# Optimization experiments

Measured on AMD Instinct MI355X. Metric: run time of the kernel, lower is better.

Reference implementation:

```python
import jax, jax.numpy as jnp
import numpy as np

N = 100_000   # nodes
E = 1_600_000 # edges (avg degree 16)
D0, D1, D2 = 128, 64, 64


def _linp(key, n_out, n_in):
    kw, kb = jax.random.split(key)
    s = 1.0 / np.sqrt(n_in)
    W = jax.random.uniform(kw, (n_out, n_in), jnp.float32, -s, s)
    b = jax.random.uniform(kb, (n_out,), jnp.float32, -s, s)
    return W, b


def setup_inputs() -> dict:
    key = jax.random.key(0)
    ks = jax.random.split(key, 9)
    h = jax.random.normal(ks[0], (N, D0), jnp.float32)
    # guarantee every row has at least one edge (avoids empty-row softmax / 0-std NaNs)
    rows = jnp.concatenate([jnp.arange(N, dtype=jnp.int32),
                            jax.random.randint(ks[1], (E - N,), 0, N, jnp.int32)])
    cols = jax.random.randint(ks[2], (E,), 0, N, jnp.int32)
    edge_index = jnp.stack([rows, cols])  # [2, E], row = softmax segment
    W11, b11 = _linp(ks[3], D1, D0)
    W12, b12 = _linp(ks[4], 1, D1)
    W13, b13 = _linp(ks[5], D1, D0)
    W21, b21 = _linp(ks[6], D2, D1)
    W22, b22 = _linp(ks[7], 1, D2)
    W23, b23 = _linp(ks[8], D2, D1)
    return dict(h=h, edge_index=edge_index,
                W11=W11, b11=b11, W12=W12, b12=b12, W13=W13, b13=b13,
                W21=W21, b21=b21, W22=W22, b22=b22, W23=W23, b23=b23)


def reference(h, edge_index, W11, b11, W12, b12, W13, b13,
              W21, b21, W22, b22, W23, b23):
    src, dst = edge_index[0], edge_index[1]

    def gat_layer(x, Wa, ba, We, be, Wv, bv):
        a = jnp.tanh(x @ Wa.T + ba)                       # [N, d] node scores (l11/l21)
        e = jnp.tanh((a[src] + a[dst]) @ We.T + be)[:, 0] # [E] per-edge logit (l12/l22)
        # per-row (segment) softmax over src = row index
        m = jax.ops.segment_max(e, src, num_segments=N)
        ex = jnp.exp(e - m[src])
        denom = jax.ops.segment_sum(ex, src, num_segments=N)
        att = ex / denom[src]                             # [E]
        v = jnp.tanh(x @ Wv.T + bv)                       # [N, d] values (l13/l23)
        out = jax.ops.segment_sum(att[:, None] * v[dst], src, num_segments=N)  # sparse mm
        return out / jnp.std(out, -1, keepdims=True, ddof=1)  # torch.std is unbiased

    h = gat_layer(h, W11, b11, W12, b12, W13, b13)
    h = gat_layer(h, W21, b21, W22, b22, W23, b23)
    return h
```

## Files before the change

kernel.cpp:

```cpp
#include <hip/hip_runtime.h>


#define WS_ALIGN 256
#define BIN_SHIFT 7
#define BIN_NODES 128
#define BIN_CAP 2560
#define MAX_BINS 1024
#define EPB 4096

typedef __attribute__((ext_vector_type(8))) short short8;
typedef __attribute__((ext_vector_type(4))) float f32x4;

__device__ __forceinline__ float wave_sum(float x) {
#pragma unroll
  for (int m = 32; m > 0; m >>= 1) x += __shfl_xor(x, m, 64);
  return x;
}

__device__ __forceinline__ float fast_tanh(float x) {
  x = fminf(15.f, fmaxf(-15.f, x));
  float e = __expf(2.f * x);
  return (e - 1.f) * __builtin_amdgcn_rcpf(e + 1.f);
}

__device__ __forceinline__ unsigned short f32_to_bf16_rne(float f) {
  unsigned u = __float_as_uint(f);
  unsigned r = u + 0x7fffu + ((u >> 16) & 1u);
  return (unsigned short)(r >> 16);
}

__device__ __forceinline__ void prepw_one(const float* __restrict__ Wa,
                                          const float* __restrict__ Wv,
                                          short* __restrict__ Wh, short* __restrict__ Wl,
                                          int K, int i) {
  int KBLK = K / 32;
  int j = i & 7;
  int c = (i >> 3) & 15;
  int q = (i >> 7) & 3;
  int r = i >> 9;
  int nt = r / KBLK, kb = r - nt * KBLK;
  int row = nt * 16 + c;
  int col = kb * 32 + q * 8 + j;
  float f = (row < 64) ? Wa[row * K + col] : Wv[(row - 64) * K + col];
  unsigned u = __float_as_uint(f);
  float hf = __uint_as_float(u & 0xffff0000u);
  Wh[i] = (short)(u >> 16);
  Wl[i] = (short)(__float_as_uint(f - hf) >> 16);
}

__global__ void k_setup(const float* __restrict__ W11, const float* __restrict__ W13,
                        short* __restrict__ Wh1, short* __restrict__ Wl1,
                        const float* __restrict__ W21, const float* __restrict__ W23,
                        short* __restrict__ Wh2, short* __restrict__ Wl2,
                        int* __restrict__ cursor, int nb) {
  int i = blockIdx.x * 256 + threadIdx.x;
  if (i < 16384) {
    prepw_one(W11, W13, Wh1, Wl1, 128, i);
  } else if (i < 16384 + 8192) {
    prepw_one(W21, W23, Wh2, Wl2, 64, i - 16384);
  } else {
    int b = i - 24576;
    if (b < nb) cursor[b] = b * BIN_CAP;
  }
}

__global__ __launch_bounds__(256) void k_bin(const int* __restrict__ src,
                                             const int* __restrict__ dst,
                                             int* __restrict__ cursor,
                                             int* __restrict__ binned, int E, int nb) {
  __shared__ int ssrc[EPB];
  __shared__ int sdst[EPB];
  __shared__ int hist[MAX_BINS];
  __shared__ int base[MAX_BINS];
  int t = threadIdx.x;
  for (int i = t; i < nb; i += 256) hist[i] = 0;
  __syncthreads();
  int e0 = blockIdx.x * EPB;
  for (int i = t; i < EPB; i += 256) {
    int e = e0 + i;
    int sv = -1, dv = 0;
    if (e < E) {
      sv = src[e];
      dv = dst[e];
      atomicAdd(&hist[sv >> BIN_SHIFT], 1);
    }
    ssrc[i] = sv;
    sdst[i] = dv;
  }
  __syncthreads();
  for (int b = t; b < nb; b += 256) {
    int c = hist[b];
    base[b] = c ? atomicAdd(&cursor[b], c) : 0;
    hist[b] = 0;
  }
  __syncthreads();
  for (int i = t; i < EPB; i += 256) {
    int sv = ssrc[i];
    if (sv >= 0) {
      int b = sv >> BIN_SHIFT;
      int r = atomicAdd(&hist[b], 1);
      int pos = base[b] + r;
      if (pos < (b + 1) * BIN_CAP)
        binned[pos] = (sdst[i] << BIN_SHIFT) | (sv & (BIN_NODES - 1));
    }
  }
}

__global__ __launch_bounds__(256) void k_sort_bin(int* __restrict__ binned,
                                                  const int* __restrict__ cursor,
                                                  int* __restrict__ rs,
                                                  int* __restrict__ re, int n) {
  __shared__ int ents[BIN_CAP];
  __shared__ int sorted[BIN_CAP];
  __shared__ int hist[BIN_NODES];
  __shared__ int scan[BIN_NODES];
  __shared__ int cur[BIN_NODES];
  int bin = blockIdx.x;
  int t = threadIdx.x;
  int nbase = bin << BIN_SHIFT;
  int cnt = cursor[bin] - bin * BIN_CAP;
  if (cnt > BIN_CAP) cnt = BIN_CAP;
  if (t < BIN_NODES) hist[t] = 0;
  __syncthreads();
  int* bp = binned + (size_t)bin * BIN_CAP;
  for (int i = t; i < cnt; i += 256) {
    int pk = bp[i];
    ents[i] = pk;
    atomicAdd(&hist[pk & (BIN_NODES - 1)], 1);
  }
  __syncthreads();
  if (t < BIN_NODES) scan[t] = hist[t];
  __syncthreads();
  for (int off = 1; off < BIN_NODES; off <<= 1) {
    int add = (t < BIN_NODES && t >= off) ? scan[t - off] : 0;
    __syncthreads();
    if (t < BIN_NODES) scan[t] += add;
    __syncthreads();
  }
  if (t < BIN_NODES) {
    int ex = scan[t] - hist[t];
    cur[t] = ex;
    int node = nbase + t;
    if (node < n) {
      rs[node] = bin * BIN_CAP + ex;
      re[node] = bin * BIN_CAP + ex + hist[t];
    }
  }
  __syncthreads();
  for (int i = t; i < cnt; i += 256) {
    int pk = ents[i];
    int pos = atomicAdd(&cur[pk & (BIN_NODES - 1)], 1);
    sorted[pos] = pk;
  }
  __syncthreads();
  for (int i = t; i < cnt; i += 256) {
    int pk = sorted[i];
    int node = pk & (BIN_NODES - 1);
    int hi = scan[node];
    int lo = hi - hist[node];
    int r = lo;
    for (int j = lo; j < hi; j++) {
      int pj = sorted[j];
      r += (pj < pk) || (pj == pk && j < i);
    }
    ents[r] = pk >> BIN_SHIFT;
  }
  __syncthreads();
  for (int i = t; i < cnt; i += 256) bp[i] = ents[i];
}

template <int K>
__global__ __launch_bounds__(256) void k_node(
    const float* __restrict__ x, const short* __restrict__ Wh,
    const short* __restrict__ Wl, const float* __restrict__ ba,
    const float* __restrict__ we, const float* __restrict__ bv,
    unsigned short* __restrict__ v_out, float* __restrict__ s_out, int n) {
  constexpr int KBLK = K / 32;
  constexpr int KP = K + 4;
  __shared__ float sx[64 * KP];
  int t = threadIdx.x;
  int l = t & 63;
  int w = t >> 6;
  int q = l >> 4, c = l & 15;
  int node0b = blockIdx.x * 64;

  {
    const float4* xg = (const float4*)(x + (size_t)node0b * K);
    constexpr int R4 = K / 4;
#pragma unroll
    for (int it = 0; it < 64 * R4 / 256; it++) {
      int i = it * 256 + t;
      int r = i / R4, k4 = i - r * R4;
      float4 val = (node0b + r < n) ? xg[i] : (float4){0.f, 0.f, 0.f, 0.f};
      *(float4*)&sx[r * KP + k4 * 4] = val;
    }
  }
  __syncthreads();

  int node0w = node0b + w * 16;
  if (node0w >= n) return;

  const short8* WhF = (const short8*)Wh;
  const short8* WlF = (const short8*)Wl;

  f32x4 acc[8];
#pragma unroll
  for (int i = 0; i < 8; i++) acc[i] = (f32x4){0.f, 0.f, 0.f, 0.f};

  const float* xl = sx + (w * 16 + c) * KP;

#pragma unroll 1
  for (int kb = 0; kb < KBLK; kb++) {
    float4 x0 = *(const float4*)&xl[kb * 32 + q * 8];
    float4 x1 = *(const float4*)&xl[kb * 32 + q * 8 + 4];
    float xv[8] = {x0.x, x0.y, x0.z, x0.w, x1.x, x1.y, x1.z, x1.w};
    short8 ah, al;
#pragma unroll
    for (int j = 0; j < 8; j++) {
      unsigned u = __float_as_uint(xv[j]);
      ah[j] = (short)(u >> 16);
      float hf = __uint_as_float(u & 0xffff0000u);
      al[j] = (short)(__float_as_uint(xv[j] - hf) >> 16);
    }
#pragma unroll
    for (int nt = 0; nt < 8; nt++) {
      short8 wh = WhF[(size_t)(nt * KBLK + kb) * 64 + l];
      short8 wl = WlF[(size_t)(nt * KBLK + kb) * 64 + l];
      acc[nt] = __builtin_amdgcn_mfma_f32_16x16x32_bf16(ah, wh, acc[nt], 0, 0, 0);
      acc[nt] = __builtin_amdgcn_mfma_f32_16x16x32_bf16(ah, wl, acc[nt], 0, 0, 0);
      acc[nt] = __builtin_amdgcn_mfma_f32_16x16x32_bf16(al, wh, acc[nt], 0, 0, 0);
    }
  }

  float p[4] = {0.f, 0.f, 0.f, 0.f};
#pragma unroll
  for (int nt = 0; nt < 4; nt++) {
    int o = nt * 16 + c;
    float bav = ba[o], wev = we[o];
#pragma unroll
    for (int r = 0; r < 4; r++) p[r] += fast_tanh(acc[nt][r] + bav) * wev;
  }
#pragma unroll
  for (int mm = 1; mm < 16; mm <<= 1) {
#pragma unroll
    for (int r = 0; r < 4; r++) p[r] += __shfl_xor(p[r], mm, 64);
  }
  if (c == 0) {
#pragma unroll
    for (int r = 0; r < 4; r++) {
      int node = node0w + q * 4 + r;
      if (node < n) s_out[node] = p[r];
    }
  }
#pragma unroll
  for (int nt = 4; nt < 8; nt++) {
    int o = (nt - 4) * 16 + c;
    float bvv = bv[o];
#pragma unroll
    for (int r = 0; r < 4; r++) {
      int node = node0w + q * 4 + r;
      if (node < n)
        v_out[(size_t)node * 64 + o] = f32_to_bf16_rne(fast_tanh(acc[nt][r] + bvv));
    }
  }
}

__global__ __launch_bounds__(256) void k_aggr(const int* __restrict__ rs,
                                              const int* __restrict__ re,
                                              const int* __restrict__ col,
                                              const float* __restrict__ s,
                                              const float* __restrict__ be_p,
                                              const unsigned short* __restrict__ v,
                                              float* __restrict__ out, int n) {
  int gw = (int)((blockIdx.x * 256 + threadIdx.x) >> 6);
  int l = threadIdx.x & 63;
  if (gw >= n) return;
  int e0 = rs[gw], e1 = re[gw];
  float srow = s[gw];
  float be = be_p[0];
  int es = l >> 4;
  int g = l & 15;
  float a0 = 0.f, a1 = 0.f, a2 = 0.f, a3 = 0.f;
  float denom = 0.f;

  for (int base = e0; base < e1; base += 64) {
    int m = e1 - base;
    if (m > 64) m = 64;
    int c = 0;
    float w = 0.f;
    if (l < m) {
      c = col[base + l];
      w = __expf(fast_tanh(srow + s[c] + be));
    }
    denom += wave_sum(w);
    int iters = (m + 3) >> 2;
    for (int it = 0; it < iters; it++) {
      int j = (it << 2) + es;
      int cj = __shfl(c, j);
      float wj = __shfl(w, j);
      uint2 pk = *(const uint2*)(v + ((size_t)cj << 6) + (g << 2));
      a0 = fmaf(wj, __uint_as_float(pk.x << 16), a0);
      a1 = fmaf(wj, __uint_as_float(pk.x & 0xffff0000u), a1);
      a2 = fmaf(wj, __uint_as_float(pk.y << 16), a2);
      a3 = fmaf(wj, __uint_as_float(pk.y & 0xffff0000u), a3);
    }
  }

#pragma unroll
  for (int mm = 16; mm < 64; mm <<= 1) {
    a0 += __shfl_xor(a0, mm, 64);
    a1 += __shfl_xor(a1, mm, 64);
    a2 += __shfl_xor(a2, mm, 64);
    a3 += __shfl_xor(a3, mm, 64);
  }
  float inv = __builtin_amdgcn_rcpf(denom);
  float o0 = a0 * inv, o1 = a1 * inv, o2 = a2 * inv, o3 = a3 * inv;
  float ls = wave_sum(o0 + o1 + o2 + o3) * 0.25f;
  float lq = wave_sum(o0 * o0 + o1 * o1 + o2 * o2 + o3 * o3) * 0.25f;
  float var = (lq - ls * ls * (1.0f / 64.f)) * (1.0f / 63.f);
  float isd = __builtin_amdgcn_rsqf(var);
  if (es == 0) {
    float4 r = {o0 * isd, o1 * isd, o2 * isd, o3 * isd};
    *(float4*)&out[(size_t)gw * 64 + (g << 2)] = r;
  }
}

extern "C" void kernel_launch(void* const* d_in, const int* in_sizes, int n_in,
                              void* d_out, int out_size, void* d_ws, size_t ws_size,
                              hipStream_t stream) {
  const float* h = (const float*)d_in[0];
  const int* ei = (const int*)d_in[1];
  const float* W11 = (const float*)d_in[2];
  const float* b11 = (const float*)d_in[3];
  const float* W12 = (const float*)d_in[4];
  const float* b12 = (const float*)d_in[5];
  const float* W13 = (const float*)d_in[6];
  const float* b13 = (const float*)d_in[7];
  const float* W21 = (const float*)d_in[8];
  const float* b21 = (const float*)d_in[9];
  const float* W22 = (const float*)d_in[10];
  const float* b22 = (const float*)d_in[11];
  const float* W23 = (const float*)d_in[12];
  const float* b23 = (const float*)d_in[13];

  const int N = in_sizes[0] / 128;
  const int E = in_sizes[1] / 2;
  const int* src = ei;
  const int* dst = ei + E;
  const int NB = (N + BIN_NODES - 1) >> BIN_SHIFT;

  char* p = (char*)d_ws;
  auto alloc = [&](size_t bytes) -> void* {
    void* r = (void*)p;
    p += (bytes + WS_ALIGN - 1) / WS_ALIGN * WS_ALIGN;
    return r;
  };
  int* cursor = (int*)alloc((size_t)NB * 4);
  int* binned = (int*)alloc((size_t)NB * BIN_CAP * 4);
  int* rsb = (int*)alloc((size_t)N * 4);
  int* reb = (int*)alloc((size_t)N * 4);
  float* sbuf = (float*)alloc((size_t)N * 4);
  unsigned short* vbuf = (unsigned short*)alloc((size_t)N * 64 * 2);
  float* out1 = (float*)alloc((size_t)N * 64 * 4);
  short* Wh1 = (short*)alloc(128 * 128 * 2);
  short* Wl1 = (short*)alloc(128 * 128 * 2);
  short* Wh2 = (short*)alloc(128 * 64 * 2);
  short* Wl2 = (short*)alloc(128 * 64 * 2);

  k_setup<<<(24576 + NB + 255) / 256, 256, 0, stream>>>(
      W11, W13, Wh1, Wl1, W21, W23, Wh2, Wl2, cursor, NB);

  k_bin<<<(E + EPB - 1) / EPB, 256, 0, stream>>>(src, dst, cursor, binned, E, NB);
  k_sort_bin<<<NB, 256, 0, stream>>>(binned, cursor, rsb, reb, N);

  k_node<128><<<(N + 63) / 64, 256, 0, stream>>>(h, Wh1, Wl1, b11, W12, b13, vbuf, sbuf, N);
  k_aggr<<<(N * 64 + 255) / 256, 256, 0, stream>>>(rsb, reb, binned, sbuf, b12, vbuf, out1, N);

  k_node<64><<<(N + 63) / 64, 256, 0, stream>>>(out1, Wh2, Wl2, b21, W22, b23, vbuf, sbuf, N);
  k_aggr<<<(N * 64 + 255) / 256, 256, 0, stream>>>(rsb, reb, binned, sbuf, b22, vbuf, (float*)d_out, N);
}
```

Measured before the change: 316.2 us.

## Store value vectors as fp32 and unroll aggregation to two edges per step

The node kernel now writes the tanh value vectors as fp32 instead of bf16, and the aggregation kernel gathers them with float4 loads. Each inner iteration handles two edges per lane group, so more gathers are in flight. The per-chunk denominator reduction moves to a single reduction at the end, and the std reduction shrinks to a 16-lane butterfly. The cost is double the bytes per gathered row and a larger value buffer, traded for less unpacking and more memory-level parallelism.

After: 324.9 us. 1.03x slower.

```diff
diff --git a/kernel.cpp b/kernel.cpp
--- a/kernel.cpp
+++ b/kernel.cpp
@@ -21,12 +21,6 @@
   x = fminf(15.f, fmaxf(-15.f, x));
   float e = __expf(2.f * x);
   return (e - 1.f) * __builtin_amdgcn_rcpf(e + 1.f);
-}
-
-__device__ __forceinline__ unsigned short f32_to_bf16_rne(float f) {
-  unsigned u = __float_as_uint(f);
-  unsigned r = u + 0x7fffu + ((u >> 16) & 1u);
-  return (unsigned short)(r >> 16);
 }
 
 __device__ __forceinline__ void prepw_one(const float* __restrict__ Wa,
@@ -174,7 +168,7 @@
     const float* __restrict__ x, const short* __restrict__ Wh,
     const short* __restrict__ Wl, const float* __restrict__ ba,
     const float* __restrict__ we, const float* __restrict__ bv,
-    unsigned short* __restrict__ v_out, float* __restrict__ s_out, int n) {
+    float* __restrict__ v_out, float* __restrict__ s_out, int n) {
   constexpr int KBLK = K / 32;
   constexpr int KP = K + 4;
   __shared__ float sx[64 * KP];
@@ -260,7 +254,7 @@
     for (int r = 0; r < 4; r++) {
       int node = node0w + q * 4 + r;
       if (node < n)
-        v_out[(size_t)node * 64 + o] = f32_to_bf16_rne(fast_tanh(acc[nt][r] + bvv));
+        v_out[(size_t)node * 64 + o] = fast_tanh(acc[nt][r] + bvv);
     }
   }
 }
@@ -270,7 +264,7 @@
                                               const int* __restrict__ col,
                                               const float* __restrict__ s,
                                               const float* __restrict__ be_p,
-                                              const unsigned short* __restrict__ v,
+                                              const float* __restrict__ v,
                                               float* __restrict__ out, int n) {
   int gw = (int)((blockIdx.x * 256 + threadIdx.x) >> 6);
   int l = threadIdx.x & 63;
@@ -281,28 +275,34 @@
   int es = l >> 4;
   int g = l & 15;
   float a0 = 0.f, a1 = 0.f, a2 = 0.f, a3 = 0.f;
-  float denom = 0.f;
+  float dl = 0.f;
 
   for (int base = e0; base < e1; base += 64) {
     int m = e1 - base;
     if (m > 64) m = 64;
+    bool act = (l < m);
     int c = 0;
-    float w = 0.f;
-    if (l < m) {
-      c = col[base + l];
-      w = __expf(fast_tanh(srow + s[c] + be));
-    }
-    denom += wave_sum(w);
-    int iters = (m + 3) >> 2;
+    if (act) c = col[base + l];
+    float sc = act ? s[c] : 0.f;
+    float w = act ? __expf(fast_tanh(srow + sc + be)) : 0.f;
+    dl += w;
+    int iters = (m + 7) >> 3;
     for (int it = 0; it < iters; it++) {
-      int j = (it << 2) + es;
-      int cj = __shfl(c, j);
-      float wj = __shfl(w, j);
-      uint2 pk = *(const uint2*)(v + ((size_t)cj << 6) + (g << 2));
-      a0 = fmaf(wj, __uint_as_float(pk.x << 16), a0);
-      a1 = fmaf(wj, __uint_as_float(pk.x & 0xffff0000u), a1);
-      a2 = fmaf(wj, __uint_as_float(pk.y << 16), a2);
-      a3 = fmaf(wj, __uint_as_float(pk.y & 0xffff0000u), a3);
+      int j0 = (it << 3) + es;
+      int c0 = __shfl(c, j0);
+      int c1 = __shfl(c, j0 + 4);
+      float4 p0 = *(const float4*)(v + ((size_t)c0 << 6) + (g << 2));
+      float4 p1 = *(const float4*)(v + ((size_t)c1 << 6) + (g << 2));
+      float w0 = __shfl(w, j0);
+      float w1 = __shfl(w, j0 + 4);
+      a0 = fmaf(w0, p0.x, a0);
+      a1 = fmaf(w0, p0.y, a1);
+      a2 = fmaf(w0, p0.z, a2);
+      a3 = fmaf(w0, p0.w, a3);
+      a0 = fmaf(w1, p1.x, a0);
+      a1 = fmaf(w1, p1.y, a1);
+      a2 = fmaf(w1, p1.z, a2);
+      a3 = fmaf(w1, p1.w, a3);
     }
   }
 
@@ -313,11 +313,17 @@
     a2 += __shfl_xor(a2, mm, 64);
     a3 += __shfl_xor(a3, mm, 64);
   }
+  float denom = wave_sum(dl);
   float inv = __builtin_amdgcn_rcpf(denom);
   float o0 = a0 * inv, o1 = a1 * inv, o2 = a2 * inv, o3 = a3 * inv;
-  float ls = wave_sum(o0 + o1 + o2 + o3) * 0.25f;
-  float lq = wave_sum(o0 * o0 + o1 * o1 + o2 * o2 + o3 * o3) * 0.25f;
-  float var = (lq - ls * ls * (1.0f / 64.f)) * (1.0f / 63.f);
+  float t0 = o0 + o1 + o2 + o3;
+  float t1 = o0 * o0 + o1 * o1 + o2 * o2 + o3 * o3;
+#pragma unroll
+  for (int mm = 1; mm < 16; mm <<= 1) {
+    t0 += __shfl_xor(t0, mm, 64);
+    t1 += __shfl_xor(t1, mm, 64);
+  }
+  float var = (t1 - t0 * t0 * (1.0f / 64.f)) * (1.0f / 63.f);
   float isd = __builtin_amdgcn_rsqf(var);
   if (es == 0) {
     float4 r = {o0 * isd, o1 * isd, o2 * isd, o3 * isd};
@@ -360,7 +366,7 @@
   int* rsb = (int*)alloc((size_t)N * 4);
   int* reb = (int*)alloc((size_t)N * 4);
   float* sbuf = (float*)alloc((size_t)N * 4);
-  unsigned short* vbuf = (unsigned short*)alloc((size_t)N * 64 * 2);
+  float* vbuf = (float*)alloc((size_t)N * 64 * 4);
   float* out1 = (float*)alloc((size_t)N * 64 * 4);
   short* Wh1 = (short*)alloc(128 * 128 * 2);
   short* Wl1 = (short*)alloc(128 * 128 * 2);
```

## Process four rows per wavefront in aggregation with grid-stride persistent blocks

Applied to the files above, without the earlier changes.

The aggregation kernel now assigns four graph rows to each wavefront, one per 16-lane quarter, instead of one row per full wave. Each quarter loads 16 edges at a time and broadcasts them within the quarter in a fully unrolled 16-step loop. The launch becomes a fixed grid of persistent blocks that grid-stride over row groups. The goal is to reduce per-row reduction and shuffle overhead and idle lanes for low-degree rows (average 16), and to put more independent gathers in flight. The cost is divergence when rows in a wave differ in degree, plus padded iterations for edges past the row end, which still issue masked gathers of row 0.

Result: faster. 286.5 us (-9.4%).

```diff
diff --git a/kernel.cpp b/kernel.cpp
--- a/kernel.cpp
+++ b/kernel.cpp
@@ -7,15 +7,10 @@
 #define BIN_CAP 2560
 #define MAX_BINS 1024
 #define EPB 4096
+#define AGGR_BLOCKS 2048
 
 typedef __attribute__((ext_vector_type(8))) short short8;
 typedef __attribute__((ext_vector_type(4))) float f32x4;
-
-__device__ __forceinline__ float wave_sum(float x) {
-#pragma unroll
-  for (int m = 32; m > 0; m >>= 1) x += __shfl_xor(x, m, 64);
-  return x;
-}
 
 __device__ __forceinline__ float fast_tanh(float x) {
   x = fminf(15.f, fmaxf(-15.f, x));
@@ -272,56 +267,60 @@
                                               const float* __restrict__ be_p,
                                               const unsigned short* __restrict__ v,
                                               float* __restrict__ out, int n) {
-  int gw = (int)((blockIdx.x * 256 + threadIdx.x) >> 6);
+  int wid = (int)((blockIdx.x * 256 + threadIdx.x) >> 6);
+  int nw = AGGR_BLOCKS * 4;
   int l = threadIdx.x & 63;
-  if (gw >= n) return;
-  int e0 = rs[gw], e1 = re[gw];
-  float srow = s[gw];
+  int q = l >> 4;
+  int g = l & 15;
+  int qb = l & 48;
   float be = be_p[0];
-  int es = l >> 4;
-  int g = l & 15;
-  float a0 = 0.f, a1 = 0.f, a2 = 0.f, a3 = 0.f;
-  float denom = 0.f;
-
-  for (int base = e0; base < e1; base += 64) {
-    int m = e1 - base;
-    if (m > 64) m = 64;
-    int c = 0;
-    float w = 0.f;
-    if (l < m) {
-      c = col[base + l];
-      w = __expf(fast_tanh(srow + s[c] + be));
-    }
-    denom += wave_sum(w);
-    int iters = (m + 3) >> 2;
-    for (int it = 0; it < iters; it++) {
-      int j = (it << 2) + es;
-      int cj = __shfl(c, j);
-      float wj = __shfl(w, j);
-      uint2 pk = *(const uint2*)(v + ((size_t)cj << 6) + (g << 2));
-      a0 = fmaf(wj, __uint_as_float(pk.x << 16), a0);
-      a1 = fmaf(wj, __uint_as_float(pk.x & 0xffff0000u), a1);
-      a2 = fmaf(wj, __uint_as_float(pk.y << 16), a2);
-      a3 = fmaf(wj, __uint_as_float(pk.y & 0xffff0000u), a3);
-    }
-  }
-
-#pragma unroll
-  for (int mm = 16; mm < 64; mm <<= 1) {
-    a0 += __shfl_xor(a0, mm, 64);
-    a1 += __shfl_xor(a1, mm, 64);
-    a2 += __shfl_xor(a2, mm, 64);
-    a3 += __shfl_xor(a3, mm, 64);
-  }
-  float inv = __builtin_amdgcn_rcpf(denom);
-  float o0 = a0 * inv, o1 = a1 * inv, o2 = a2 * inv, o3 = a3 * inv;
-  float ls = wave_sum(o0 + o1 + o2 + o3) * 0.25f;
-  float lq = wave_sum(o0 * o0 + o1 * o1 + o2 * o2 + o3 * o3) * 0.25f;
-  float var = (lq - ls * ls * (1.0f / 64.f)) * (1.0f / 63.f);
-  float isd = __builtin_amdgcn_rsqf(var);
-  if (es == 0) {
-    float4 r = {o0 * isd, o1 * isd, o2 * isd, o3 * isd};
-    *(float4*)&out[(size_t)gw * 64 + (g << 2)] = r;
+  int ngroups = (n + 3) >> 2;
+
+  for (int grp = wid; grp < ngroups; grp += nw) {
+    int node = grp * 4 + q;
+    bool vn = node < n;
+    int e0 = vn ? rs[node] : 0;
+    int e1 = vn ? re[node] : 0;
+    float srow = vn ? s[node] : 0.f;
+    float a0 = 0.f, a1 = 0.f, a2 = 0.f, a3 = 0.f;
+    float dl = 0.f;
+
+    for (int cb = 0;; cb += 16) {
+      int rem = e1 - e0 - cb;
+      if (__all(rem <= 0)) break;
+      bool act = g < rem;
+      int c = act ? col[e0 + cb + g] : 0;
+      float w = act ? __expf(fast_tanh(srow + s[c] + be)) : 0.f;
+      dl += w;
+#pragma unroll
+      for (int jj = 0; jj < 16; jj++) {
+        int cj = __shfl(c, qb + jj, 64);
+        float wj = __shfl(w, qb + jj, 64);
+        uint2 pk = *(const uint2*)(v + ((size_t)cj << 6) + (g << 2));
+        a0 = fmaf(wj, __uint_as_float(pk.x << 16), a0);
+        a1 = fmaf(wj, __uint_as_float(pk.x & 0xffff0000u), a1);
+        a2 = fmaf(wj, __uint_as_float(pk.y << 16), a2);
+        a3 = fmaf(wj, __uint_as_float(pk.y & 0xffff0000u), a3);
+      }
+    }
+
+#pragma unroll
+    for (int mm = 1; mm < 16; mm <<= 1) dl += __shfl_xor(dl, mm, 64);
+    float inv = __builtin_amdgcn_rcpf(dl);
+    float o0 = a0 * inv, o1 = a1 * inv, o2 = a2 * inv, o3 = a3 * inv;
+    float t0 = o0 + o1 + o2 + o3;
+    float t1 = o0 * o0 + o1 * o1 + o2 * o2 + o3 * o3;
+#pragma unroll
+    for (int mm = 1; mm < 16; mm <<= 1) {
+      t0 += __shfl_xor(t0, mm, 64);
+      t1 += __shfl_xor(t1, mm, 64);
+    }
+    float var = (t1 - t0 * t0 * (1.0f / 64.f)) * (1.0f / 63.f);
+    float isd = __builtin_amdgcn_rsqf(var);
+    if (vn) {
+      float4 r = {o0 * isd, o1 * isd, o2 * isd, o3 * isd};
+      *(float4*)&out[(size_t)node * 64 + (g << 2)] = r;
+    }
   }
 }
 
@@ -374,8 +373,8 @@
   k_sort_bin<<<NB, 256, 0, stream>>>(binned, cursor, rsb, reb, N);
 
   k_node<128><<<(N + 63) / 64, 256, 0, stream>>>(h, Wh1, Wl1, b11, W12, b13, vbuf, sbuf, N);
-  k_aggr<<<(N * 64 + 255) / 256, 256, 0, stream>>>(rsb, reb, binned, sbuf, b12, vbuf, out1, N);
+  k_aggr<<<AGGR_BLOCKS, 256, 0, stream>>>(rsb, reb, binned, sbuf, b12, vbuf, out1, N);
 
   k_node<64><<<(N + 63) / 64, 256, 0, stream>>>(out1, Wh2, Wl2, b21, W22, b23, vbuf, sbuf, N);
-  k_aggr<<<(N * 64 + 255) / 256, 256, 0, stream>>>(rsb, reb, binned, sbuf, b22, vbuf, (float*)d_out, N);
-}
+  k_aggr<<<AGGR_BLOCKS, 256, 0, stream>>>(rsb, reb, binned, sbuf, b22, vbuf, (float*)d_out, N);
+}
```
